# Performance work log

Hardware: AMD Instinct MI355X
Metric: run time of the kernel (lower is better)

Reference implementation:

```python
import jax, jax.numpy as jnp
import numpy as np


def _conv1d_same(seq, w, b):
    # seq: (N, 1, C), w: (1, 1, K) odd K, bias (1,). SAME padding, stride 1.
    k = w.shape[-1]
    p = (k - 1) // 2
    out = jax.lax.conv_general_dilated(
        seq, w, window_strides=(1,), padding=[(p, p)],
        dimension_numbers=("NCH", "OIH", "NCH"))
    return out + b[None, :, None]


def setup_inputs() -> dict:
    key = jax.random.key(0)
    k1, k2, k3 = jax.random.split(key, 3)
    N, C, H, W = 32, 512, 32, 32
    x = jax.random.normal(k1, (N, C, H, W), dtype=jnp.float32)
    wq = jax.random.normal(k2, (1, 1, 5), dtype=jnp.float32) * 0.2
    bq = jax.random.normal(k3, (1,), dtype=jnp.float32) * 0.1
    return {"x": x, "wq": wq, "bq": bq}


def reference(x, wq, bq):
    N, C, H, W = x.shape
    # Global average pool over spatial dims -> (N, 1, C)
    gap = jnp.mean(x, axis=(2, 3)).reshape(N, 1, C)
    # NOTE: original module applies conv_q to BOTH query and key (conv_k unused)
    query = jax.nn.sigmoid(_conv1d_same(gap, wq, bq))          # (N, 1, C)
    key_t = jnp.transpose(query, (0, 2, 1))                    # (N, C, 1)
    # Outer product key @ query -> (N, C, C), softmax over flattened C*C
    qk = jnp.einsum("nci,nij->ncj", key_t, query)              # (N, C, C)
    qk = jax.nn.softmax(qk.reshape(N, C * C), axis=-1).reshape(N, C, C)
    # value: (N, H*W, C)
    value = jnp.transpose(x, (0, 2, 3, 1)).reshape(N, H * W, C)
    att = jnp.einsum("npc,ncd->npd", value, qk)                # (N, HW, C)
    att = jnp.transpose(att, (0, 2, 1)).reshape(N, C, H, W)
    return x * att
```

## Files before the change

kernel.cpp:

```cpp
#include <hip/hip_runtime.h>
#include <math.h>

#define NB 32
#define CC 512
#define HW 1024
#define NJ 10

__device__ __forceinline__ float wave_reduce(float s) {
#pragma unroll
  for (int off = 32; off; off >>= 1) s += __shfl_down(s, off, 64);
  return s;
}

__global__ __launch_bounds__(256) void k_gap(const float* __restrict__ x,
                                             float* __restrict__ gap) {
  int wv = threadIdx.x >> 6, lane = threadIdx.x & 63;
  int r0 = blockIdx.x * 16;
#pragma unroll
  for (int it = 0; it < 4; ++it) {
    int row = r0 + wv * 4 + it;
    const float4* xp = (const float4*)x + (size_t)row * 256;
    float s = 0.f;
#pragma unroll
    for (int k = 0; k < 4; ++k) {
      float4 v = xp[lane + 64 * k];
      s += v.x + v.y + v.z + v.w;
    }
    s = wave_reduce(s);
    if (lane == 0) gap[row] = s * (1.0f / 1024.0f);
  }
}

__global__ __launch_bounds__(512) void k_fused(const float* __restrict__ x,
                                               const float* __restrict__ gap,
                                               const float* __restrict__ wq,
                                               const float* __restrict__ bq,
                                               float* __restrict__ out) {
  int n = blockIdx.x >> 4, pblk = blockIdx.x & 15;
  int t = threadIdx.x;
  int cg = t >> 4, pg = t & 15;
  int wv = t >> 6, lane = t & 63;

  __shared__ float qs[CC];
  __shared__ float wred[8][NJ];
  __shared__ float4 sred[8][16][NJ + 1];
  __shared__ float4 sfin[16][NJ + 1];
  __shared__ float invZ_sh;

  const float cj[NJ] = {1.f, 1.f, 0.5f, 1.f / 6.f, 1.f / 24.f, 1.f / 120.f,
                        1.f / 720.f, 1.f / 5040.f, 1.f / 40320.f, 1.f / 362880.f};

  float4 xv[16];
  const float4* x4 = (const float4*)x;
  size_t base = (size_t)(n * CC + cg * 16) * 256 + (size_t)pblk * 16 + pg;
#pragma unroll
  for (int i = 0; i < 16; ++i) xv[i] = x4[base + (size_t)i * 256];

  {
    int c = t;
    const float* g = gap + n * CC;
    float z = bq[0];
#pragma unroll
    for (int k = 0; k < 5; ++k) {
      int idx = c + k - 2;
      float gv = (idx >= 0 && idx < CC) ? g[idx] : 0.f;
      z = fmaf(gv, wq[k], z);
    }
    float qv = 1.f / (1.f + expf(-z));
    qs[c] = qv;
    float pj[NJ];
    float pw = 1.f;
#pragma unroll
    for (int j = 0; j < NJ; ++j) { pj[j] = pw; pw *= qv; }
#pragma unroll
    for (int j = 0; j < NJ; ++j) pj[j] = wave_reduce(pj[j]);
    if (lane == 0) {
#pragma unroll
      for (int j = 0; j < NJ; ++j) wred[wv][j] = pj[j];
    }
  }
  __syncthreads();
  if (t == 0) {
    float Z = 0.f;
#pragma unroll
    for (int j = 0; j < NJ; ++j) {
      float P = 0.f;
#pragma unroll
      for (int w8 = 0; w8 < 8; ++w8) P += wred[w8][j];
      Z = fmaf(cj[j] * P, P, Z);
    }
    invZ_sh = 1.f / Z;
  }

  float4 acc[NJ];
#pragma unroll
  for (int j = 0; j < NJ; ++j) acc[j] = make_float4(0.f, 0.f, 0.f, 0.f);
#pragma unroll
  for (int i = 0; i < 16; ++i) {
    float qc = qs[cg * 16 + i];
    float4 v = xv[i];
    float w = 1.f;
#pragma unroll
    for (int j = 0; j < NJ; ++j) {
      acc[j].x = fmaf(w, v.x, acc[j].x);
      acc[j].y = fmaf(w, v.y, acc[j].y);
      acc[j].z = fmaf(w, v.z, acc[j].z);
      acc[j].w = fmaf(w, v.w, acc[j].w);
      w *= qc;
    }
  }
#pragma unroll
  for (int j = 0; j < NJ; ++j) {
    acc[j].x += __shfl_xor(acc[j].x, 16, 64);
    acc[j].y += __shfl_xor(acc[j].y, 16, 64);
    acc[j].z += __shfl_xor(acc[j].z, 16, 64);
    acc[j].w += __shfl_xor(acc[j].w, 16, 64);
    acc[j].x += __shfl_xor(acc[j].x, 32, 64);
    acc[j].y += __shfl_xor(acc[j].y, 32, 64);
    acc[j].z += __shfl_xor(acc[j].z, 32, 64);
    acc[j].w += __shfl_xor(acc[j].w, 32, 64);
  }
  if (lane < 16) {
#pragma unroll
    for (int j = 0; j < NJ; ++j) sred[wv][lane][j] = acc[j];
  }
  __syncthreads();
  if (t < 160) {
    int pp = t / NJ, j = t - pp * NJ;
    float4 a = make_float4(0.f, 0.f, 0.f, 0.f);
#pragma unroll
    for (int w8 = 0; w8 < 8; ++w8) {
      float4 v = sred[w8][pp][j];
      a.x += v.x; a.y += v.y; a.z += v.z; a.w += v.w;
    }
    float sc = cj[j] * invZ_sh;
    a.x *= sc; a.y *= sc; a.z *= sc; a.w *= sc;
    sfin[pp][j] = a;
  }
  __syncthreads();

  float4 sj[NJ];
#pragma unroll
  for (int j = 0; j < NJ; ++j) sj[j] = sfin[pg][j];
  float4* o4 = (float4*)out;
#pragma unroll
  for (int i = 0; i < 16; ++i) {
    float qd = qs[cg * 16 + i];
    float w = 1.f;
    float4 att = make_float4(0.f, 0.f, 0.f, 0.f);
#pragma unroll
    for (int j = 0; j < NJ; ++j) {
      att.x = fmaf(w, sj[j].x, att.x);
      att.y = fmaf(w, sj[j].y, att.y);
      att.z = fmaf(w, sj[j].z, att.z);
      att.w = fmaf(w, sj[j].w, att.w);
      w *= qd;
    }
    float4 xvv = xv[i];
    float4 o;
    o.x = xvv.x * att.x; o.y = xvv.y * att.y;
    o.z = xvv.z * att.z; o.w = xvv.w * att.w;
    o4[base + (size_t)i * 256] = o;
  }
}

extern "C" void kernel_launch(void* const* d_in, const int* in_sizes, int n_in,
                              void* d_out, int out_size, void* d_ws, size_t ws_size,
                              hipStream_t stream) {
  const float* x  = (const float*)d_in[0];
  const float* wq = (const float*)d_in[1];
  const float* bq = (const float*)d_in[2];
  float* out = (float*)d_out;
  float* gap = (float*)d_ws;

  k_gap<<<NB * CC / 16, 256, 0, stream>>>(x, gap);
  k_fused<<<NB * 16, 512, 0, stream>>>(x, gap, wq, bq, out);
}
```

Before: 131.3 us.

## Fuse GAP and attention into one cooperative kernel with grid sync

Replaces the separate global-average-pool kernel and the fused attention kernel with a single cooperative kernel. Each block loads its slice of x into registers once, computes partial per-channel sums, writes them to workspace, then does a grid-wide sync before reducing the partials and doing the softmax/power-series attention. This removes the second full read of x and one kernel launch, but adds a grid barrier and needs all 512 blocks co-resident. The power-series accumulation is also split into two halves of five terms to lower register pressure, with a fallback to the old two-kernel path if occupancy is too low.

```diff
diff --git a/kernel.cpp b/kernel.cpp
--- a/kernel.cpp
+++ b/kernel.cpp
@@ -1,5 +1,8 @@
 #include <hip/hip_runtime.h>
+#include <hip/hip_cooperative_groups.h>
 #include <math.h>
+
+namespace cg = cooperative_groups;
 
 #define NB 32
 #define CC 512
@@ -10,6 +13,174 @@
 #pragma unroll
   for (int off = 32; off; off >>= 1) s += __shfl_down(s, off, 64);
   return s;
+}
+
+__global__ __launch_bounds__(512, 4) void k_onepass(
+    const float* __restrict__ x, const float* __restrict__ wq,
+    const float* __restrict__ bq, float* __restrict__ out,
+    float* __restrict__ gpart) {
+  int b = blockIdx.x;
+  int n = b >> 4;
+  int t = threadIdx.x;
+  int cg = t >> 4, pg = t & 15;
+  int wv = t >> 6, lane = t & 63;
+
+  __shared__ float gs[CC];
+  __shared__ float qs[CC];
+  __shared__ float wred[8][NJ];
+  __shared__ float4 sred[8][16][NJ + 1];
+  __shared__ float4 sfin[16][NJ + 1];
+  __shared__ float invZ_sh;
+
+  const float cj[NJ] = {1.f, 1.f, 0.5f, 1.f / 6.f, 1.f / 24.f, 1.f / 120.f,
+                        1.f / 720.f, 1.f / 5040.f, 1.f / 40320.f, 1.f / 362880.f};
+
+  float4 xv[16];
+  const float4* x4 = (const float4*)x;
+  size_t base = (size_t)(n * CC + cg * 16) * 256 + (size_t)(b & 15) * 16 + pg;
+#pragma unroll
+  for (int i = 0; i < 16; ++i) xv[i] = x4[base + (size_t)i * 256];
+
+  {
+    float ps[16];
+#pragma unroll
+    for (int i = 0; i < 16; ++i) {
+      float4 v = xv[i];
+      ps[i] = v.x + v.y + v.z + v.w;
+    }
+#pragma unroll
+    for (int off = 1; off < 16; off <<= 1) {
+#pragma unroll
+      for (int i = 0; i < 16; ++i) ps[i] += __shfl_xor(ps[i], off, 64);
+    }
+    if (pg == 0) {
+#pragma unroll
+      for (int i = 0; i < 16; ++i) gs[cg * 16 + i] = ps[i];
+    }
+  }
+  __syncthreads();
+  if (t < 128) ((float4*)&gpart[(size_t)b * CC])[t] = ((const float4*)gs)[t];
+
+  cg::this_grid().sync();
+
+  {
+    int c = t;
+    float g = 0.f;
+#pragma unroll
+    for (int pb = 0; pb < 16; ++pb) g += gpart[(size_t)(n * 16 + pb) * CC + c];
+    gs[c] = g * (1.0f / 1024.0f);
+  }
+  __syncthreads();
+  {
+    int c = t;
+    float z = bq[0];
+#pragma unroll
+    for (int k = 0; k < 5; ++k) {
+      int idx = c + k - 2;
+      float gv = (idx >= 0 && idx < CC) ? gs[idx] : 0.f;
+      z = fmaf(gv, wq[k], z);
+    }
+    float qv = 1.f / (1.f + expf(-z));
+    qs[c] = qv;
+    float pj[NJ];
+    float pw = 1.f;
+#pragma unroll
+    for (int j = 0; j < NJ; ++j) { pj[j] = pw; pw *= qv; }
+#pragma unroll
+    for (int j = 0; j < NJ; ++j) pj[j] = wave_reduce(pj[j]);
+    if (lane == 0) {
+#pragma unroll
+      for (int j = 0; j < NJ; ++j) wred[wv][j] = pj[j];
+    }
+  }
+  __syncthreads();
+  if (t == 0) {
+    float Z = 0.f;
+#pragma unroll
+    for (int j = 0; j < NJ; ++j) {
+      float P = 0.f;
+#pragma unroll
+      for (int w8 = 0; w8 < 8; ++w8) P += wred[w8][j];
+      Z = fmaf(cj[j] * P, P, Z);
+    }
+    invZ_sh = 1.f / Z;
+  }
+
+#pragma unroll
+  for (int half = 0; half < 2; ++half) {
+    float4 acc[5];
+#pragma unroll
+    for (int j = 0; j < 5; ++j) acc[j] = make_float4(0.f, 0.f, 0.f, 0.f);
+#pragma unroll
+    for (int i = 0; i < 16; ++i) {
+      float qc = qs[cg * 16 + i];
+      float4 v = xv[i];
+      float w;
+      if (half == 0) w = 1.f;
+      else { float q2 = qc * qc; w = q2 * q2 * qc; }
+#pragma unroll
+      for (int j = 0; j < 5; ++j) {
+        acc[j].x = fmaf(w, v.x, acc[j].x);
+        acc[j].y = fmaf(w, v.y, acc[j].y);
+        acc[j].z = fmaf(w, v.z, acc[j].z);
+        acc[j].w = fmaf(w, v.w, acc[j].w);
+        w *= qc;
+      }
+    }
+#pragma unroll
+    for (int j = 0; j < 5; ++j) {
+      acc[j].x += __shfl_xor(acc[j].x, 16, 64);
+      acc[j].y += __shfl_xor(acc[j].y, 16, 64);
+      acc[j].z += __shfl_xor(acc[j].z, 16, 64);
+      acc[j].w += __shfl_xor(acc[j].w, 16, 64);
+      acc[j].x += __shfl_xor(acc[j].x, 32, 64);
+      acc[j].y += __shfl_xor(acc[j].y, 32, 64);
+      acc[j].z += __shfl_xor(acc[j].z, 32, 64);
+      acc[j].w += __shfl_xor(acc[j].w, 32, 64);
+    }
+    if (lane < 16) {
+#pragma unroll
+      for (int j = 0; j < 5; ++j) sred[wv][lane][half * 5 + j] = acc[j];
+    }
+  }
+  __syncthreads();
+  if (t < 160) {
+    int pp = t / NJ, j = t - pp * NJ;
+    float4 a = make_float4(0.f, 0.f, 0.f, 0.f);
+#pragma unroll
+    for (int w8 = 0; w8 < 8; ++w8) {
+      float4 v = sred[w8][pp][j];
+      a.x += v.x; a.y += v.y; a.z += v.z; a.w += v.w;
+    }
+    float sc = cj[j] * invZ_sh;
+    a.x *= sc; a.y *= sc; a.z *= sc; a.w *= sc;
+    sfin[pp][j] = a;
+  }
+  __syncthreads();
+
+  float4 sj[NJ];
+#pragma unroll
+  for (int j = 0; j < NJ; ++j) sj[j] = sfin[pg][j];
+  float4* o4 = (float4*)out;
+#pragma unroll
+  for (int i = 0; i < 16; ++i) {
+    float qd = qs[cg * 16 + i];
+    float w = 1.f;
+    float4 att = make_float4(0.f, 0.f, 0.f, 0.f);
+#pragma unroll
+    for (int j = 0; j < NJ; ++j) {
+      att.x = fmaf(w, sj[j].x, att.x);
+      att.y = fmaf(w, sj[j].y, att.y);
+      att.z = fmaf(w, sj[j].z, att.z);
+      att.w = fmaf(w, sj[j].w, att.w);
+      w *= qd;
+    }
+    float4 xvv = xv[i];
+    float4 o;
+    o.x = xvv.x * att.x; o.y = xvv.y * att.y;
+    o.z = xvv.z * att.z; o.w = xvv.w * att.w;
+    o4[base + (size_t)i * 256] = o;
+  }
 }
 
 __global__ __launch_bounds__(256) void k_gap(const float* __restrict__ x,
@@ -171,8 +342,18 @@
   const float* wq = (const float*)d_in[1];
   const float* bq = (const float*)d_in[2];
   float* out = (float*)d_out;
-  float* gap = (float*)d_ws;
-
-  k_gap<<<NB * CC / 16, 256, 0, stream>>>(x, gap);
-  k_fused<<<NB * 16, 512, 0, stream>>>(x, gap, wq, bq, out);
-}
+  float* gpart = (float*)d_ws;
+
+  int maxB = 0;
+  (void)hipOccupancyMaxActiveBlocksPerMultiprocessor(&maxB, (const void*)k_onepass,
+                                                     512, 0);
+  if (maxB >= 2) {
+    void* args[] = {(void*)&x, (void*)&wq, (void*)&bq, (void*)&out, (void*)&gpart};
+    hipLaunchCooperativeKernel((const void*)k_onepass, dim3(NB * 16), dim3(512),
+                               args, 0, stream);
+  } else {
+    float* gap = gpart;
+    k_gap<<<NB * CC / 16, 256, 0, stream>>>(x, gap);
+    k_fused<<<NB * 16, 512, 0, stream>>>(x, gap, wq, bq, out);
+  }
+}
```

After: 132.9 us. No clear change (+1.2%).

## Split q/normalizer into separate kernel and halve accumulator registers in output kernel

Applied to the files above, without the earlier changes.

Moves the sigmoid/conv and softmax-normalizer computation out of the per-tile fused kernel into a small per-batch kernel, so it is no longer recomputed by each of 16 blocks per sample. The output kernel now takes precomputed q and coefficients, splits the 10-term accumulation into two halves of 5 to cut register pressure, and sets launch bounds for 2 blocks per CU. The GAP kernel also issues all loads before reducing, to raise memory-level parallelism. This adds an extra kernel launch and a global round-trip for q, and the two-pass accumulation re-reads xv and qs.

```diff
diff --git a/kernel.cpp b/kernel.cpp
--- a/kernel.cpp
+++ b/kernel.cpp
@@ -3,7 +3,6 @@
 
 #define NB 32
 #define CC 512
-#define HW 1024
 #define NJ 10
 
 __device__ __forceinline__ float wave_reduce(float s) {
@@ -15,114 +14,133 @@
 __global__ __launch_bounds__(256) void k_gap(const float* __restrict__ x,
                                              float* __restrict__ gap) {
   int wv = threadIdx.x >> 6, lane = threadIdx.x & 63;
-  int r0 = blockIdx.x * 16;
+  int r0 = blockIdx.x * 16 + wv * 4;
+  float4 v[4][4];
 #pragma unroll
   for (int it = 0; it < 4; ++it) {
-    int row = r0 + wv * 4 + it;
-    const float4* xp = (const float4*)x + (size_t)row * 256;
+    const float4* xp = (const float4*)x + (size_t)(r0 + it) * 256;
+#pragma unroll
+    for (int k = 0; k < 4; ++k) v[it][k] = xp[lane + 64 * k];
+  }
+#pragma unroll
+  for (int it = 0; it < 4; ++it) {
     float s = 0.f;
 #pragma unroll
-    for (int k = 0; k < 4; ++k) {
-      float4 v = xp[lane + 64 * k];
-      s += v.x + v.y + v.z + v.w;
-    }
+    for (int k = 0; k < 4; ++k)
+      s += v[it][k].x + v[it][k].y + v[it][k].z + v[it][k].w;
     s = wave_reduce(s);
-    if (lane == 0) gap[row] = s * (1.0f / 1024.0f);
-  }
-}
-
-__global__ __launch_bounds__(512) void k_fused(const float* __restrict__ x,
-                                               const float* __restrict__ gap,
-                                               const float* __restrict__ wq,
-                                               const float* __restrict__ bq,
-                                               float* __restrict__ out) {
+    if (lane == 0) gap[r0 + it] = s * (1.0f / 1024.0f);
+  }
+}
+
+__global__ __launch_bounds__(512) void k_q(const float* __restrict__ gap,
+                                           const float* __restrict__ wq,
+                                           const float* __restrict__ bq,
+                                           float* __restrict__ q,
+                                           float* __restrict__ coef) {
+  int n = blockIdx.x, c = threadIdx.x;
+  int wv = c >> 6, lane = c & 63;
+  __shared__ float wred[8][NJ];
+  const float cj[NJ] = {1.f, 1.f, 0.5f, 1.f / 6.f, 1.f / 24.f, 1.f / 120.f,
+                        1.f / 720.f, 1.f / 5040.f, 1.f / 40320.f, 1.f / 362880.f};
+  const float* g = gap + n * CC;
+  float z = bq[0];
+#pragma unroll
+  for (int k = 0; k < 5; ++k) {
+    int idx = c + k - 2;
+    float gv = (idx >= 0 && idx < CC) ? g[idx] : 0.f;
+    z = fmaf(gv, wq[k], z);
+  }
+  float qv = 1.f / (1.f + expf(-z));
+  q[n * CC + c] = qv;
+  float pj[NJ];
+  float pw = 1.f;
+#pragma unroll
+  for (int j = 0; j < NJ; ++j) { pj[j] = pw; pw *= qv; }
+#pragma unroll
+  for (int j = 0; j < NJ; ++j) pj[j] = wave_reduce(pj[j]);
+  if (lane == 0) {
+#pragma unroll
+    for (int j = 0; j < NJ; ++j) wred[wv][j] = pj[j];
+  }
+  __syncthreads();
+  if (c == 0) {
+    float Z = 0.f;
+    float P[NJ];
+#pragma unroll
+    for (int j = 0; j < NJ; ++j) {
+      float p = 0.f;
+#pragma unroll
+      for (int w8 = 0; w8 < 8; ++w8) p += wred[w8][j];
+      P[j] = p;
+      Z = fmaf(cj[j] * p, p, Z);
+    }
+    float iz = 1.f / Z;
+#pragma unroll
+    for (int j = 0; j < NJ; ++j) coef[n * NJ + j] = cj[j] * iz;
+  }
+}
+
+__global__ __launch_bounds__(512, 2) void k_out(const float* __restrict__ x,
+                                                const float* __restrict__ q,
+                                                const float* __restrict__ coef,
+                                                float* __restrict__ out) {
   int n = blockIdx.x >> 4, pblk = blockIdx.x & 15;
   int t = threadIdx.x;
   int cg = t >> 4, pg = t & 15;
   int wv = t >> 6, lane = t & 63;
 
   __shared__ float qs[CC];
-  __shared__ float wred[8][NJ];
+  __shared__ float cf[NJ];
   __shared__ float4 sred[8][16][NJ + 1];
   __shared__ float4 sfin[16][NJ + 1];
-  __shared__ float invZ_sh;
-
-  const float cj[NJ] = {1.f, 1.f, 0.5f, 1.f / 6.f, 1.f / 24.f, 1.f / 120.f,
-                        1.f / 720.f, 1.f / 5040.f, 1.f / 40320.f, 1.f / 362880.f};
+
+  qs[t] = q[n * CC + t];
+  if (t < NJ) cf[t] = coef[n * NJ + t];
 
   float4 xv[16];
   const float4* x4 = (const float4*)x;
   size_t base = (size_t)(n * CC + cg * 16) * 256 + (size_t)pblk * 16 + pg;
 #pragma unroll
   for (int i = 0; i < 16; ++i) xv[i] = x4[base + (size_t)i * 256];
-
-  {
-    int c = t;
-    const float* g = gap + n * CC;
-    float z = bq[0];
-#pragma unroll
-    for (int k = 0; k < 5; ++k) {
-      int idx = c + k - 2;
-      float gv = (idx >= 0 && idx < CC) ? g[idx] : 0.f;
-      z = fmaf(gv, wq[k], z);
-    }
-    float qv = 1.f / (1.f + expf(-z));
-    qs[c] = qv;
-    float pj[NJ];
-    float pw = 1.f;
-#pragma unroll
-    for (int j = 0; j < NJ; ++j) { pj[j] = pw; pw *= qv; }
-#pragma unroll
-    for (int j = 0; j < NJ; ++j) pj[j] = wave_reduce(pj[j]);
-    if (lane == 0) {
-#pragma unroll
-      for (int j = 0; j < NJ; ++j) wred[wv][j] = pj[j];
-    }
-  }
-  __syncthreads();
-  if (t == 0) {
-    float Z = 0.f;
-#pragma unroll
-    for (int j = 0; j < NJ; ++j) {
-      float P = 0.f;
-#pragma unroll
-      for (int w8 = 0; w8 < 8; ++w8) P += wred[w8][j];
-      Z = fmaf(cj[j] * P, P, Z);
-    }
-    invZ_sh = 1.f / Z;
-  }
-
-  float4 acc[NJ];
-#pragma unroll
-  for (int j = 0; j < NJ; ++j) acc[j] = make_float4(0.f, 0.f, 0.f, 0.f);
-#pragma unroll
-  for (int i = 0; i < 16; ++i) {
-    float qc = qs[cg * 16 + i];
-    float4 v = xv[i];
-    float w = 1.f;
-#pragma unroll
-    for (int j = 0; j < NJ; ++j) {
-      acc[j].x = fmaf(w, v.x, acc[j].x);
-      acc[j].y = fmaf(w, v.y, acc[j].y);
-      acc[j].z = fmaf(w, v.z, acc[j].z);
-      acc[j].w = fmaf(w, v.w, acc[j].w);
-      w *= qc;
-    }
-  }
-#pragma unroll
-  for (int j = 0; j < NJ; ++j) {
-    acc[j].x += __shfl_xor(acc[j].x, 16, 64);
-    acc[j].y += __shfl_xor(acc[j].y, 16, 64);
-    acc[j].z += __shfl_xor(acc[j].z, 16, 64);
-    acc[j].w += __shfl_xor(acc[j].w, 16, 64);
-    acc[j].x += __shfl_xor(acc[j].x, 32, 64);
-    acc[j].y += __shfl_xor(acc[j].y, 32, 64);
-    acc[j].z += __shfl_xor(acc[j].z, 32, 64);
-    acc[j].w += __shfl_xor(acc[j].w, 32, 64);
-  }
-  if (lane < 16) {
-#pragma unroll
-    for (int j = 0; j < NJ; ++j) sred[wv][lane][j] = acc[j];
+  __syncthreads();
+
+#pragma unroll
+  for (int half = 0; half < 2; ++half) {
+    float4 acc[5];
+#pragma unroll
+    for (int j = 0; j < 5; ++j) acc[j] = make_float4(0.f, 0.f, 0.f, 0.f);
+#pragma unroll
+    for (int i = 0; i < 16; ++i) {
+      float qc = qs[cg * 16 + i];
+      float4 v = xv[i];
+      float w;
+      if (half == 0) w = 1.f;
+      else { float q2 = qc * qc; w = q2 * q2 * qc; }
+#pragma unroll
+      for (int j = 0; j < 5; ++j) {
+        acc[j].x = fmaf(w, v.x, acc[j].x);
+        acc[j].y = fmaf(w, v.y, acc[j].y);
+        acc[j].z = fmaf(w, v.z, acc[j].z);
+        acc[j].w = fmaf(w, v.w, acc[j].w);
+        w *= qc;
+      }
+    }
+#pragma unroll
+    for (int j = 0; j < 5; ++j) {
+      acc[j].x += __shfl_xor(acc[j].x, 16, 64);
+      acc[j].y += __shfl_xor(acc[j].y, 16, 64);
+      acc[j].z += __shfl_xor(acc[j].z, 16, 64);
+      acc[j].w += __shfl_xor(acc[j].w, 16, 64);
+      acc[j].x += __shfl_xor(acc[j].x, 32, 64);
+      acc[j].y += __shfl_xor(acc[j].y, 32, 64);
+      acc[j].z += __shfl_xor(acc[j].z, 32, 64);
+      acc[j].w += __shfl_xor(acc[j].w, 32, 64);
+    }
+    if (lane < 16) {
+#pragma unroll
+      for (int j = 0; j < 5; ++j) sred[wv][lane][half * 5 + j] = acc[j];
+    }
   }
   __syncthreads();
   if (t < 160) {
@@ -133,7 +151,7 @@
       float4 v = sred[w8][pp][j];
       a.x += v.x; a.y += v.y; a.z += v.z; a.w += v.w;
     }
-    float sc = cj[j] * invZ_sh;
+    float sc = cf[j];
     a.x *= sc; a.y *= sc; a.z *= sc; a.w *= sc;
     sfin[pp][j] = a;
   }
@@ -171,8 +189,13 @@
   const float* wq = (const float*)d_in[1];
   const float* bq = (const float*)d_in[2];
   float* out = (float*)d_out;
-  float* gap = (float*)d_ws;
+  char* ws = (char*)d_ws;
+
+  float* gap  = (float*)(ws);
+  float* q    = (float*)(ws + 65536);
+  float* coef = (float*)(ws + 131072);
 
   k_gap<<<NB * CC / 16, 256, 0, stream>>>(x, gap);
-  k_fused<<<NB * 16, 512, 0, stream>>>(x, gap, wq, bq, out);
-}
+  k_q<<<NB, 512, 0, stream>>>(gap, wq, bq, q, coef);
+  k_out<<<NB * 16, 512, 0, stream>>>(x, q, coef, out);
+}
```

New measurement: 132.5 us. Within noise of the previous version (+0.9%).
